# Kernel tuning notes

Measured on AMD Instinct MI355X. Metric: run time of the kernel, lower is better.

The kernel has to match this reference:

```python
import jax, jax.numpy as jnp
import numpy as np

N_NODES = 100000
N_EDGES = 6400000
D_FEAT = 8
# Fuzzy inference system: 3 Gaussian membership functions per input
# (negative / zero / positive linguistic terms), 3x3 = 9 rules per edge.
MF_CENTERS = jnp.array([-1.0, 0.0, 1.0], dtype=jnp.float32)
MF_SIGMA = 0.5


def setup_inputs() -> dict:
    key = jax.random.key(0)
    k1, k2, k3, k4 = jax.random.split(key, 4)
    feat = jax.random.normal(k1, (N_NODES, D_FEAT), dtype=jnp.float32)
    edge_src = jax.random.randint(k2, (N_EDGES,), 0, N_NODES, dtype=jnp.int32)
    edge_dst = jax.random.randint(k3, (N_EDGES,), 0, N_NODES, dtype=jnp.int32)
    etypes = jax.random.randint(k4, (N_EDGES,), 0, 4, dtype=jnp.int32)
    return {"feat": feat, "edge_src": edge_src, "edge_dst": edge_dst, "etypes": etypes}


def _ante_generator(h_src, h_dst):
    # Relative-coordinate antecedent inputs (first two feature dims are coords).
    x1 = h_dst[:, 0] - h_src[:, 0]  # [E]
    x2 = h_dst[:, 1] - h_src[:, 1]  # [E]
    return x1, x2


def _fuzzy_infer_sys(x1, x2):
    inv2s2 = 1.0 / (2.0 * MF_SIGMA * MF_SIGMA)
    mu1 = jnp.exp(-((x1[:, None] - MF_CENTERS) ** 2) * inv2s2)  # [E, 3]
    mu2 = jnp.exp(-((x2[:, None] - MF_CENTERS) ** 2) * inv2s2)  # [E, 3]
    # Rule firing strengths: outer product of memberships -> [E, 9]
    ante = (mu1[:, :, None] * mu2[:, None, :]).reshape(-1, 9)
    return ante


def reference(feat, edge_src, edge_dst, etypes):
    # apply_edges: gather src/dst node features per edge
    h_src = feat[edge_src]  # [E, D]
    h_dst = feat[edge_dst]  # [E, D]
    x1, x2 = _ante_generator(h_src, h_dst)
    ante = _fuzzy_infer_sys(x1, x2)  # [E, 9] stored in g.edata['ante']
    return ante
```

## Files before the change

### kernel.cpp

```cpp
#include <hip/hip_runtime.h>


#define TPB 256

__global__ __launch_bounds__(TPB) void ante_kernel(
    const float* __restrict__ feat,
    const int*   __restrict__ esrc,
    const int*   __restrict__ edst,
    float*       __restrict__ out,
    int e4,
    int nf4)
{
    __shared__ float4 lds4[TPB * 9];
    const int tid = threadIdx.x;
    const int t   = blockIdx.x * TPB + tid;

    if (t < e4) {
        const int4 s4 = reinterpret_cast<const int4*>(esrc)[t];
        const int4 d4 = reinterpret_cast<const int4*>(edst)[t];
        const int ss[4] = {s4.x, s4.y, s4.z, s4.w};
        const int dd[4] = {d4.x, d4.y, d4.z, d4.w};

        float res[36];
#pragma unroll
        for (int q = 0; q < 4; ++q) {
            const float2 fs = *reinterpret_cast<const float2*>(feat + (size_t)ss[q] * 8);
            const float2 fd = *reinterpret_cast<const float2*>(feat + (size_t)dd[q] * 8);
            const float x1 = fd.x - fs.x;
            const float x2 = fd.y - fs.y;

            float m1[3], m2[3];
            {
                const float a = x1 + 1.0f, c = x1 - 1.0f;
                m1[0] = __expf(-2.0f * a * a);
                m1[1] = __expf(-2.0f * x1 * x1);
                m1[2] = __expf(-2.0f * c * c);
            }
            {
                const float a = x2 + 1.0f, c = x2 - 1.0f;
                m2[0] = __expf(-2.0f * a * a);
                m2[1] = __expf(-2.0f * x2 * x2);
                m2[2] = __expf(-2.0f * c * c);
            }
#pragma unroll
            for (int i = 0; i < 3; ++i)
#pragma unroll
                for (int j = 0; j < 3; ++j)
                    res[q * 9 + i * 3 + j] = m1[i] * m2[j];
        }

        float4* my4 = &lds4[tid * 9];
#pragma unroll
        for (int k = 0; k < 9; ++k) {
            float4 v;
            v.x = res[k * 4 + 0];
            v.y = res[k * 4 + 1];
            v.z = res[k * 4 + 2];
            v.w = res[k * 4 + 3];
            my4[k] = v;
        }
    }
    __syncthreads();

    const size_t blk_f4 = (size_t)blockIdx.x * (TPB * 9);
    float4* out4 = reinterpret_cast<float4*>(out);

#pragma unroll
    for (int k = 0; k < 9; ++k) {
        const int f = k * TPB + tid;
        const size_t g = blk_f4 + (size_t)f;
        if (g < (size_t)nf4) out4[g] = lds4[f];
    }
}

extern "C" void kernel_launch(void* const* d_in, const int* in_sizes, int n_in,
                              void* d_out, int out_size, void* d_ws, size_t ws_size,
                              hipStream_t stream) {
    const float* feat = (const float*)d_in[0];
    const int*   esrc = (const int*)d_in[1];
    const int*   edst = (const int*)d_in[2];
    float* out = (float*)d_out;

    const int E   = in_sizes[1];
    const int e4  = E / 4;
    const int nf4 = out_size / 4;
    const int grid = (e4 + TPB - 1) / TPB;
    ante_kernel<<<grid, TPB, 0, stream>>>(feat, esrc, edst, out, e4, nf4);
}
```

Measured before the change: 97.98 us.

## Process two edges per thread with nontemporal loads/stores and higher occupancy

```diff
diff --git a/kernel.cpp b/kernel.cpp
--- a/kernel.cpp
+++ b/kernel.cpp
@@ -3,31 +3,36 @@
 
 #define TPB 256
 
-__global__ __launch_bounds__(TPB) void ante_kernel(
+typedef float  f2 __attribute__((ext_vector_type(2)));
+typedef float  f4 __attribute__((ext_vector_type(4)));
+typedef int    i2 __attribute__((ext_vector_type(2)));
+
+__global__ __launch_bounds__(TPB, 8) void ante_kernel(
     const float* __restrict__ feat,
     const int*   __restrict__ esrc,
     const int*   __restrict__ edst,
     float*       __restrict__ out,
-    int e4,
+    int e2,
     int nf4)
 {
-    __shared__ float4 lds4[TPB * 9];
+    __shared__ float lds[TPB * 18];
     const int tid = threadIdx.x;
     const int t   = blockIdx.x * TPB + tid;
 
-    if (t < e4) {
-        const int4 s4 = reinterpret_cast<const int4*>(esrc)[t];
-        const int4 d4 = reinterpret_cast<const int4*>(edst)[t];
-        const int ss[4] = {s4.x, s4.y, s4.z, s4.w};
-        const int dd[4] = {d4.x, d4.y, d4.z, d4.w};
+    if (t < e2) {
+        const i2 s2 = __builtin_nontemporal_load(reinterpret_cast<const i2*>(esrc) + t);
+        const i2 d2 = __builtin_nontemporal_load(reinterpret_cast<const i2*>(edst) + t);
 
-        float res[36];
+        const f2 fs0 = *reinterpret_cast<const f2*>(feat + (size_t)s2.x * 8);
+        const f2 fd0 = *reinterpret_cast<const f2*>(feat + (size_t)d2.x * 8);
+        const f2 fs1 = *reinterpret_cast<const f2*>(feat + (size_t)s2.y * 8);
+        const f2 fd1 = *reinterpret_cast<const f2*>(feat + (size_t)d2.y * 8);
+
+        float res[18];
 #pragma unroll
-        for (int q = 0; q < 4; ++q) {
-            const float2 fs = *reinterpret_cast<const float2*>(feat + (size_t)ss[q] * 8);
-            const float2 fd = *reinterpret_cast<const float2*>(feat + (size_t)dd[q] * 8);
-            const float x1 = fd.x - fs.x;
-            const float x2 = fd.y - fs.y;
+        for (int q = 0; q < 2; ++q) {
+            const float x1 = (q == 0) ? (fd0.x - fs0.x) : (fd1.x - fs1.x);
+            const float x2 = (q == 0) ? (fd0.y - fs0.y) : (fd1.y - fs1.y);
 
             float m1[3], m2[3];
             {
@@ -49,27 +54,27 @@
                     res[q * 9 + i * 3 + j] = m1[i] * m2[j];
         }
 
-        float4* my4 = &lds4[tid * 9];
+        f2* my2 = reinterpret_cast<f2*>(lds) + tid * 9;
 #pragma unroll
         for (int k = 0; k < 9; ++k) {
-            float4 v;
-            v.x = res[k * 4 + 0];
-            v.y = res[k * 4 + 1];
-            v.z = res[k * 4 + 2];
-            v.w = res[k * 4 + 3];
-            my4[k] = v;
+            f2 v; v.x = res[2 * k]; v.y = res[2 * k + 1];
+            my2[k] = v;
         }
     }
     __syncthreads();
 
-    const size_t blk_f4 = (size_t)blockIdx.x * (TPB * 9);
-    float4* out4 = reinterpret_cast<float4*>(out);
+    const size_t blk_f4 = (size_t)blockIdx.x * (TPB * 9 / 2);
+    f4* out4 = reinterpret_cast<f4*>(out);
+    const f4* lds4 = reinterpret_cast<const f4*>(lds);
 
 #pragma unroll
-    for (int k = 0; k < 9; ++k) {
+    for (int k = 0; k < 5; ++k) {
         const int f = k * TPB + tid;
-        const size_t g = blk_f4 + (size_t)f;
-        if (g < (size_t)nf4) out4[g] = lds4[f];
+        if (f < TPB * 9 / 2) {
+            const size_t g = blk_f4 + (size_t)f;
+            if (g < (size_t)nf4)
+                __builtin_nontemporal_store(lds4[f], out4 + g);
+        }
     }
 }
 
@@ -82,8 +87,8 @@
     float* out = (float*)d_out;
 
     const int E   = in_sizes[1];
-    const int e4  = E / 4;
+    const int e2  = E / 2;
     const int nf4 = out_size / 4;
-    const int grid = (e4 + TPB - 1) / TPB;
-    ante_kernel<<<grid, TPB, 0, stream>>>(feat, esrc, edst, out, e4, nf4);
+    const int grid = (e2 + TPB - 1) / TPB;
+    ante_kernel<<<grid, TPB, 0, stream>>>(feat, esrc, edst, out, e2, nf4);
 }
```

Result: no change. 97.28 us (median of 2 runs) (-0.7%).
